# Optimization experiments

Measured on AMD Instinct MI355X. Metric: run time of the kernel, lower is better.

The kernel has to match this reference:

```python
import jax, jax.numpy as jnp
import numpy as np
import math

D_MODEL = 1024
BATCH, SEQ = 8, 2048
EPS_ENT = 1e-10
EPS_LN = 1e-5


def setup_inputs() -> dict:
    key = jax.random.key(0)
    kq, kk, kv, kw = jax.random.split(key, 4)
    query = jax.random.normal(kq, (BATCH, SEQ, D_MODEL), dtype=jnp.float32)
    k_ = jax.random.normal(kk, (BATCH, SEQ, D_MODEL), dtype=jnp.float32)
    v_ = jax.random.normal(kv, (BATCH, SEQ, D_MODEL), dtype=jnp.float32)
    harm_w = jax.random.normal(kw, (D_MODEL, D_MODEL), dtype=jnp.float32) / math.sqrt(D_MODEL)
    harm_b = jnp.zeros((D_MODEL,), dtype=jnp.float32)
    norm_gamma = jnp.ones((D_MODEL,), dtype=jnp.float32)
    norm_beta = jnp.zeros((D_MODEL,), dtype=jnp.float32)
    return {"query": query, "key": k_, "value": v_, "harm_w": harm_w,
            "harm_b": harm_b, "norm_gamma": norm_gamma, "norm_beta": norm_beta}


def reference(query, key, value, harm_w, harm_b, norm_gamma, norm_beta):
    scale = jnp.asarray(math.sqrt(D_MODEL), dtype=query.dtype)
    # scores: [B, Sq, Sk]
    scores = jnp.einsum('bqd,bkd->bqk', query, key) / scale
    attention = jax.nn.softmax(scores, axis=-1)
    # dropout p=0 (eval/deterministic)
    # syntony stat (no-grad in original): normalized mean entropy of attention rows
    entropy = -jnp.sum(attention * jnp.log(attention + EPS_ENT), axis=-1)
    max_entropy = math.log(attention.shape[-1])
    syntony = jnp.clip(1.0 - jnp.mean(entropy) / max_entropy, 0.0, 1.0)
    # output: [B, Sq, D]
    output = jnp.einsum('bqk,bkd->bqd', attention, value)
    # harmonize: linear then syntonic norm (layernorm-style) over feature dim
    h = jnp.einsum('bqd,de->bqe', output, harm_w) + harm_b
    mu = jnp.mean(h, axis=-1, keepdims=True)
    var = jnp.var(h, axis=-1, keepdims=True)
    out = (h - mu) * jax.lax.rsqrt(var + EPS_LN) * norm_gamma + norm_beta
    return out, syntony
```

## Files before the change

kernel.cpp:

```cpp
#include <hip/hip_runtime.h>
#include <math.h>

#define D_MODEL 1024
#define SEQ 2048
#define BATCH 8
#define ROWS (BATCH*SEQ)

typedef __attribute__((ext_vector_type(8))) short bf16x8;
typedef __attribute__((ext_vector_type(4))) float f32x4;

__device__ __forceinline__ unsigned short f2bf(float f) {
  union { float f; unsigned u; } x; x.f = f;
  unsigned r = x.u + 0x7fffu + ((x.u >> 16) & 1u);
  return (unsigned short)(r >> 16);
}

__device__ __forceinline__ void gld16(const unsigned short* g, unsigned short* l) {
  __builtin_amdgcn_global_load_lds(
      (const __attribute__((address_space(1))) unsigned int*)g,
      (__attribute__((address_space(3))) unsigned int*)l, 16, 0, 0);
}

#define BAR() __builtin_amdgcn_s_barrier()
#define LDSOFF(p) ((unsigned)(size_t)(__attribute__((address_space(3))) unsigned short*)(p))

template<int EPI>
__global__ __launch_bounds__(512, 2)
void gemm_b(const unsigned short* __restrict__ A, const unsigned short* __restrict__ B,
            void* __restrict__ Cp, int lda, int ldb, int ldc, int K,
            size_t sA, size_t sB, size_t sC, float scale,
            float* __restrict__ lsum, float* __restrict__ tsum, int lstride,
            const float* __restrict__ bias)
{
  __shared__ __align__(16) unsigned short S[2][2][2][8192];
  const int tid  = threadIdx.x;
  const int lane = tid & 63;
  const int wid  = tid >> 6;
  const int quad = lane >> 4, l16 = lane & 15;
  const int wr = wid >> 2, wc = wid & 3;
  const int m0 = blockIdx.y * 256, n0 = blockIdx.x * 256;
  const int bz = blockIdx.z;

  const int sr = tid >> 2;
  const int u  = ((tid & 3) - (sr >> 1)) & 3;
  const unsigned short* Ag0 = A + (size_t)bz * sA + (size_t)(m0 + sr) * lda + u * 8;
  const unsigned short* Ag1 = Ag0 + (size_t)128 * lda;
  const unsigned short* Bg0 = B + (size_t)bz * sB + (size_t)(n0 + sr) * ldb + u * 8;
  const unsigned short* Bg1 = Bg0 + (size_t)128 * ldb;
  const int ldst = tid * 8;

  f32x4 acc[8][4];
#pragma unroll
  for (int i = 0; i < 8; i++)
#pragma unroll
    for (int j = 0; j < 4; j++) acc[i][j] = (f32x4){0.f, 0.f, 0.f, 0.f};

  const int NT = K >> 6;
  bf16x8 af[4], bfr[4];

#define STG(mat, bufp, ks, koff) do { \
    gld16(((mat) ? Bg0 : Ag0) + (koff), &S[bufp][mat][ks][ldst]); \
    gld16(((mat) ? Bg1 : Ag1) + (koff), &S[bufp][mat][ks][4096 + ldst]); \
  } while (0)

#define LOAD_A(mih, ks, P) do { \
    const int R0 = wr * 128 + (mih) * 64 + l16; \
    const int s = (quad + (R0 >> 1)) & 3; \
    const unsigned offA = LDSOFF(&S[P][0][ks][R0 * 32 + s * 8]); \
    asm volatile("ds_read_b128 %0, %1 offset:0"    : "=v"(af[0]) : "v"(offA)); \
    asm volatile("ds_read_b128 %0, %1 offset:1024" : "=v"(af[1]) : "v"(offA)); \
    asm volatile("ds_read_b128 %0, %1 offset:2048" : "=v"(af[2]) : "v"(offA)); \
    asm volatile("ds_read_b128 %0, %1 offset:3072" : "=v"(af[3]) : "v"(offA)); \
  } while (0)

#define LOAD_B(ks, P) do { \
    const int R0 = wc * 64 + l16; \
    const int s = (quad + (R0 >> 1)) & 3; \
    const unsigned offB = LDSOFF(&S[P][1][ks][R0 * 32 + s * 8]); \
    asm volatile("ds_read_b128 %0, %1 offset:0"    : "=v"(bfr[0]) : "v"(offB)); \
    asm volatile("ds_read_b128 %0, %1 offset:1024" : "=v"(bfr[1]) : "v"(offB)); \
    asm volatile("ds_read_b128 %0, %1 offset:2048" : "=v"(bfr[2]) : "v"(offB)); \
    asm volatile("ds_read_b128 %0, %1 offset:3072" : "=v"(bfr[3]) : "v"(offB)); \
  } while (0)

#define MWAIT() do { \
    asm volatile("s_waitcnt lgkmcnt(0)" ::: "memory"); \
    __builtin_amdgcn_sched_barrier(0); \
  } while (0)

#define MFMA16(mih) do { \
    _Pragma("unroll") \
    for (int i = 0; i < 4; i++) \
    _Pragma("unroll") \
    for (int j = 0; j < 4; j++) \
      acc[(mih) * 4 + i][j] = __builtin_amdgcn_mfma_f32_16x16x32_bf16( \
          af[i], bfr[j], acc[(mih) * 4 + i][j], 0, 0, 0); \
  } while (0)

#define TILE_BODY(P, v) do { \
    const int kHi = ((v) + 1) * 64 + 32; \
    const int kLo = ((v) + 2) * 64; \
     \
    LOAD_A(0, 0, P); LOAD_B(0, P); \
    if ((v) + 1 < NT) STG(0, (P) ^ 1, 1, kHi); \
    BAR(); MWAIT(); \
    __builtin_amdgcn_s_setprio(1); MFMA16(0); __builtin_amdgcn_s_setprio(0); \
    BAR(); \
     \
    LOAD_A(1, 0, P); \
    if ((v) + 1 < NT) STG(1, (P) ^ 1, 1, kHi); \
    BAR(); MWAIT(); \
    __builtin_amdgcn_s_setprio(1); MFMA16(1); __builtin_amdgcn_s_setprio(0); \
    BAR(); \
     \
    LOAD_A(0, 1, P); LOAD_B(1, P); \
    if ((v) + 2 < NT) STG(0, P, 0, kLo); \
    BAR(); MWAIT(); \
    __builtin_amdgcn_s_setprio(1); MFMA16(0); __builtin_amdgcn_s_setprio(0); \
    BAR(); \
     \
    LOAD_A(1, 1, P); \
    if ((v) + 2 < NT) STG(1, P, 0, kLo); \
    BAR(); MWAIT(); \
    __builtin_amdgcn_s_setprio(1); MFMA16(1); __builtin_amdgcn_s_setprio(0); \
     \
    if ((v) + 1 < NT) { \
      if ((v) + 2 < NT) asm volatile("s_waitcnt vmcnt(4)" ::: "memory"); \
      else              asm volatile("s_waitcnt vmcnt(0)" ::: "memory"); \
    } \
    BAR(); \
  } while (0)

  STG(0, 0, 0, 0);  STG(1, 0, 0, 0);
  STG(0, 0, 1, 32); STG(1, 0, 1, 32);
  if (NT > 1) { STG(0, 1, 0, 64); STG(1, 1, 0, 64); }

  if (NT > 1) asm volatile("s_waitcnt vmcnt(4)" ::: "memory");
  else        asm volatile("s_waitcnt vmcnt(0)" ::: "memory");
  BAR();

  for (int v = 0; v < NT; v += 2) {
    TILE_BODY(0, v);
    TILE_BODY(1, v + 1);
  }

#undef TILE_BODY
#undef STG
#undef LOAD_A
#undef LOAD_B
#undef MWAIT
#undef MFMA16

  if constexpr (EPI == 0) {
    unsigned short* C = (unsigned short*)Cp + (size_t)bz * sC;
#pragma unroll
    for (int mi = 0; mi < 8; mi++)
#pragma unroll
      for (int r = 0; r < 4; r++) {
        const int grow = m0 + wr * 128 + mi * 16 + quad * 4 + r;
#pragma unroll
        for (int ni = 0; ni < 4; ni++) {
          const int gcol = n0 + wc * 64 + ni * 16 + l16;
          C[(size_t)grow * ldc + gcol] = f2bf(acc[mi][ni][r]);
        }
      }
  } else if constexpr (EPI == 1) {
    unsigned short* C = (unsigned short*)Cp + (size_t)bz * sC;
#pragma unroll
    for (int mi = 0; mi < 8; mi++)
#pragma unroll
      for (int r = 0; r < 4; r++) {
        const int grow = m0 + wr * 128 + mi * 16 + quad * 4 + r;
        float es = 0.f, ts = 0.f;
#pragma unroll
        for (int ni = 0; ni < 4; ni++) {
          const int gcol = n0 + wc * 64 + ni * 16 + l16;
          float s = acc[mi][ni][r] * scale;
          float e = __expf(s);
          es += e; ts += s * e;
          C[(size_t)grow * ldc + gcol] = f2bf(e);
        }
#pragma unroll
        for (int off = 1; off < 16; off <<= 1) {
          es += __shfl_xor(es, off, 64);
          ts += __shfl_xor(ts, off, 64);
        }
        if (l16 == 0) {
          atomicAdd(&lsum[bz * lstride + grow], es);
          atomicAdd(&tsum[bz * lstride + grow], ts);
        }
      }
  } else {
    float* C = (float*)Cp + (size_t)bz * sC;
#pragma unroll
    for (int mi = 0; mi < 8; mi++)
#pragma unroll
      for (int r = 0; r < 4; r++) {
        const int grow = m0 + wr * 128 + mi * 16 + quad * 4 + r;
        const float linv = 1.0f / lsum[bz * lstride + grow];
#pragma unroll
        for (int ni = 0; ni < 4; ni++) {
          const int gcol = n0 + wc * 64 + ni * 16 + l16;
          C[(size_t)grow * ldc + gcol] = acc[mi][ni][r] * linv + bias[gcol];
        }
      }
  }
}

__global__ __launch_bounds__(256)
void cvt_k(const float* __restrict__ src, unsigned short* __restrict__ dst, int n8)
{
  int stride = gridDim.x * 256;
  for (int i = blockIdx.x * 256 + threadIdx.x; i < n8; i += stride) {
    const float4* s = (const float4*)(src + (size_t)i * 8);
    float4 a = s[0], b = s[1];
    union { unsigned short v[8]; uint4 u; } o;
    o.v[0] = f2bf(a.x); o.v[1] = f2bf(a.y); o.v[2] = f2bf(a.z); o.v[3] = f2bf(a.w);
    o.v[4] = f2bf(b.x); o.v[5] = f2bf(b.y); o.v[6] = f2bf(b.z); o.v[7] = f2bf(b.w);
    *(uint4*)(dst + (size_t)i * 8) = o.u;
  }
}

__global__ __launch_bounds__(256)
void wtr_k(const float* __restrict__ W, unsigned short* __restrict__ WT)
{
  __shared__ float t[32][33];
  int bx = blockIdx.x * 32, by = blockIdx.y * 32;
  int tx = threadIdx.x & 31, ty = threadIdx.x >> 5;
#pragma unroll
  for (int i = 0; i < 32; i += 8)
    t[ty + i][tx] = W[(size_t)(by + ty + i) * D_MODEL + bx + tx];
  __syncthreads();
#pragma unroll
  for (int i = 0; i < 32; i += 8)
    WT[(size_t)(bx + ty + i) * D_MODEL + by + tx] = f2bf(t[tx][ty + i]);
}

__global__ __launch_bounds__(256)
void ln_k(float* __restrict__ out, const float* __restrict__ gamma,
          const float* __restrict__ beta)
{
  const size_t row = blockIdx.x;
  float4* p = (float4*)(out + row * D_MODEL);
  const int tid = threadIdx.x;
  float4 v = p[tid];
  float s  = v.x + v.y + v.z + v.w;
  float sq = v.x * v.x + v.y * v.y + v.z * v.z + v.w * v.w;
#pragma unroll
  for (int off = 1; off < 64; off <<= 1) {
    s  += __shfl_xor(s, off, 64);
    sq += __shfl_xor(sq, off, 64);
  }
  __shared__ float sh[8];
  int wv = tid >> 6, lane = tid & 63;
  if (lane == 0) { sh[wv] = s; sh[4 + wv] = sq; }
  __syncthreads();
  s  = sh[0] + sh[1] + sh[2] + sh[3];
  sq = sh[4] + sh[5] + sh[6] + sh[7];
  float mean = s * (1.f / 1024.f);
  float var  = sq * (1.f / 1024.f) - mean * mean;
  float rstd = rsqrtf(var + 1e-5f);
  float4 g = ((const float4*)gamma)[tid];
  float4 b = ((const float4*)beta)[tid];
  v.x = (v.x - mean) * rstd * g.x + b.x;
  v.y = (v.y - mean) * rstd * g.y + b.y;
  v.z = (v.z - mean) * rstd * g.z + b.z;
  v.w = (v.w - mean) * rstd * g.w + b.w;
  p[tid] = v;
}

__global__ __launch_bounds__(256)
void syn_k(const float* __restrict__ l, const float* __restrict__ t,
           float* __restrict__ out)
{
  float s = 0.f;
  for (int r = threadIdx.x; r < ROWS; r += 256) {
    float lv = l[r];
    s += logf(lv) - t[r] / lv;
  }
#pragma unroll
  for (int off = 1; off < 64; off <<= 1) s += __shfl_xor(s, off, 64);
  __shared__ float sh[4];
  if ((threadIdx.x & 63) == 0) sh[threadIdx.x >> 6] = s;
  __syncthreads();
  if (threadIdx.x == 0) {
    float tot  = sh[0] + sh[1] + sh[2] + sh[3];
    float ment = tot / (float)ROWS;
    float syn  = 1.0f - ment / logf((float)SEQ);
    syn = fminf(fmaxf(syn, 0.f), 1.f);
    out[(size_t)ROWS * D_MODEL] = syn;
  }
}

extern "C" void kernel_launch(void* const* d_in, const int* in_sizes, int n_in,
                              void* d_out, int out_size, void* d_ws, size_t ws_size,
                              hipStream_t stream)
{
  const float* q     = (const float*)d_in[0];
  const float* k     = (const float*)d_in[1];
  const float* v     = (const float*)d_in[2];
  const float* hw    = (const float*)d_in[3];
  const float* hb    = (const float*)d_in[4];
  const float* gamma = (const float*)d_in[5];
  const float* beta  = (const float*)d_in[6];
  float* out = (float*)d_out;

  const size_t MB = 1024ull * 1024ull;
  char* ws = (char*)d_ws;
  unsigned short* P   = (unsigned short*)(ws);
  unsigned short* VWT = (unsigned short*)(ws + 64 * MB);
  float* lsum = (float*)(ws + 96 * MB);
  float* tsum = lsum + ROWS;

  unsigned short* Vb = (unsigned short*)out;
  unsigned short* WT = (unsigned short*)((char*)out + 32 * MB);
  unsigned short* Qb = (unsigned short*)out;
  unsigned short* Kb = (unsigned short*)((char*)out + 32 * MB);

  hipMemsetAsync(lsum, 0, 2 * ROWS * sizeof(float), stream);

  const int n8 = ROWS * D_MODEL / 8;

  cvt_k<<<4096, 256, 0, stream>>>(v, Vb, n8);
  wtr_k<<<dim3(32, 32), 256, 0, stream>>>(hw, WT);
  gemm_b<0><<<dim3(ROWS / 256, D_MODEL / 256, 1), 512, 0, stream>>>(
      WT, Vb, VWT, D_MODEL, D_MODEL, ROWS, D_MODEL,
      0, 0, 0, 1.f, nullptr, nullptr, 0, nullptr);

  cvt_k<<<4096, 256, 0, stream>>>(q, Qb, n8);
  cvt_k<<<4096, 256, 0, stream>>>(k, Kb, n8);
  gemm_b<1><<<dim3(SEQ / 256, SEQ / 256, BATCH), 512, 0, stream>>>(
      Qb, Kb, P, D_MODEL, D_MODEL, SEQ, D_MODEL,
      (size_t)SEQ * D_MODEL, (size_t)SEQ * D_MODEL, (size_t)SEQ * SEQ,
      0.03125f, lsum, tsum, SEQ, nullptr);

  gemm_b<2><<<dim3(D_MODEL / 256, SEQ / 256, BATCH), 512, 0, stream>>>(
      P, VWT, out, SEQ, ROWS, D_MODEL, SEQ,
      (size_t)SEQ * SEQ, (size_t)SEQ, (size_t)SEQ * D_MODEL,
      1.f, lsum, tsum, SEQ, hb);

  ln_k<<<ROWS, 256, 0, stream>>>(out, gamma, beta);
  syn_k<<<1, 256, 0, stream>>>(lsum, tsum, out);
}
```

Measured before the change: 468.3 us.

## Remap workgroups across XCDs and merge GEMM tile phases into two larger steps

Workgroup indices are remapped so consecutive tiles land on the same XCD (round-robin chunking by 8), aiming to improve L2 reuse of shared A/B panels. The tile loop now has two phases per k-tile instead of four. Each phase loads all 8 A fragments and 4 B fragments and issues 32 MFMAs, halving the barrier count. This raises register pressure (8 A fragments held at once) and shifts the global prefetch issue points, which may reduce overlap or risk spills under launch bounds of 512 threads with 2 blocks.

```diff
diff --git a/kernel.cpp b/kernel.cpp
--- a/kernel.cpp
+++ b/kernel.cpp
@@ -38,8 +38,18 @@
   const int wid  = tid >> 6;
   const int quad = lane >> 4, l16 = lane & 15;
   const int wr = wid >> 2, wc = wid & 3;
-  const int m0 = blockIdx.y * 256, n0 = blockIdx.x * 256;
-  const int bz = blockIdx.z;
+
+  int bx = blockIdx.x, by = blockIdx.y, bz = blockIdx.z;
+  {
+    const int nx = gridDim.x, ny = gridDim.y;
+    const int nwg = nx * ny * gridDim.z;
+    const int wg  = bx + nx * (by + ny * bz);
+    const int cpx = nwg >> 3;
+    int idx = (wg & 7) * cpx + (wg >> 3);
+    bx = idx % nx; idx /= nx;
+    by = idx % ny; bz = idx / ny;
+  }
+  const int m0 = by * 256, n0 = bx * 256;
 
   const int sr = tid >> 2;
   const int u  = ((tid & 3) - (sr >> 1)) & 3;
@@ -56,24 +66,28 @@
     for (int j = 0; j < 4; j++) acc[i][j] = (f32x4){0.f, 0.f, 0.f, 0.f};
 
   const int NT = K >> 6;
-  bf16x8 af[4], bfr[4];
+  bf16x8 af[8], bfr[4];
 
 #define STG(mat, bufp, ks, koff) do { \
     gld16(((mat) ? Bg0 : Ag0) + (koff), &S[bufp][mat][ks][ldst]); \
     gld16(((mat) ? Bg1 : Ag1) + (koff), &S[bufp][mat][ks][4096 + ldst]); \
   } while (0)
 
-#define LOAD_A(mih, ks, P) do { \
-    const int R0 = wr * 128 + (mih) * 64 + l16; \
+#define LOAD_A8(ks, P) do { \
+    const int R0 = wr * 128 + l16; \
     const int s = (quad + (R0 >> 1)) & 3; \
     const unsigned offA = LDSOFF(&S[P][0][ks][R0 * 32 + s * 8]); \
     asm volatile("ds_read_b128 %0, %1 offset:0"    : "=v"(af[0]) : "v"(offA)); \
     asm volatile("ds_read_b128 %0, %1 offset:1024" : "=v"(af[1]) : "v"(offA)); \
     asm volatile("ds_read_b128 %0, %1 offset:2048" : "=v"(af[2]) : "v"(offA)); \
     asm volatile("ds_read_b128 %0, %1 offset:3072" : "=v"(af[3]) : "v"(offA)); \
-  } while (0)
-
-#define LOAD_B(ks, P) do { \
+    asm volatile("ds_read_b128 %0, %1 offset:4096" : "=v"(af[4]) : "v"(offA)); \
+    asm volatile("ds_read_b128 %0, %1 offset:5120" : "=v"(af[5]) : "v"(offA)); \
+    asm volatile("ds_read_b128 %0, %1 offset:6144" : "=v"(af[6]) : "v"(offA)); \
+    asm volatile("ds_read_b128 %0, %1 offset:7168" : "=v"(af[7]) : "v"(offA)); \
+  } while (0)
+
+#define LOAD_B4(ks, P) do { \
     const int R0 = wc * 64 + l16; \
     const int s = (quad + (R0 >> 1)) & 3; \
     const unsigned offB = LDSOFF(&S[P][1][ks][R0 * 32 + s * 8]); \
@@ -88,41 +102,29 @@
     __builtin_amdgcn_sched_barrier(0); \
   } while (0)
 
-#define MFMA16(mih) do { \
+#define MFMA32() do { \
     _Pragma("unroll") \
-    for (int i = 0; i < 4; i++) \
+    for (int i = 0; i < 8; i++) \
     _Pragma("unroll") \
     for (int j = 0; j < 4; j++) \
-      acc[(mih) * 4 + i][j] = __builtin_amdgcn_mfma_f32_16x16x32_bf16( \
-          af[i], bfr[j], acc[(mih) * 4 + i][j], 0, 0, 0); \
+      acc[i][j] = __builtin_amdgcn_mfma_f32_16x16x32_bf16( \
+          af[i], bfr[j], acc[i][j], 0, 0, 0); \
   } while (0)
 
 #define TILE_BODY(P, v) do { \
     const int kHi = ((v) + 1) * 64 + 32; \
     const int kLo = ((v) + 2) * 64; \
      \
-    LOAD_A(0, 0, P); LOAD_B(0, P); \
-    if ((v) + 1 < NT) STG(0, (P) ^ 1, 1, kHi); \
+    LOAD_A8(0, P); LOAD_B4(0, P); \
+    if ((v) + 1 < NT) { STG(0, (P) ^ 1, 1, kHi); STG(1, (P) ^ 1, 1, kHi); } \
     BAR(); MWAIT(); \
-    __builtin_amdgcn_s_setprio(1); MFMA16(0); __builtin_amdgcn_s_setprio(0); \
+    __builtin_amdgcn_s_setprio(1); MFMA32(); __builtin_amdgcn_s_setprio(0); \
     BAR(); \
      \
-    LOAD_A(1, 0, P); \
-    if ((v) + 1 < NT) STG(1, (P) ^ 1, 1, kHi); \
+    LOAD_A8(1, P); LOAD_B4(1, P); \
+    if ((v) + 2 < NT) { STG(0, P, 0, kLo); STG(1, P, 0, kLo); } \
     BAR(); MWAIT(); \
-    __builtin_amdgcn_s_setprio(1); MFMA16(1); __builtin_amdgcn_s_setprio(0); \
-    BAR(); \
-     \
-    LOAD_A(0, 1, P); LOAD_B(1, P); \
-    if ((v) + 2 < NT) STG(0, P, 0, kLo); \
-    BAR(); MWAIT(); \
-    __builtin_amdgcn_s_setprio(1); MFMA16(0); __builtin_amdgcn_s_setprio(0); \
-    BAR(); \
-     \
-    LOAD_A(1, 1, P); \
-    if ((v) + 2 < NT) STG(1, P, 0, kLo); \
-    BAR(); MWAIT(); \
-    __builtin_amdgcn_s_setprio(1); MFMA16(1); __builtin_amdgcn_s_setprio(0); \
+    __builtin_amdgcn_s_setprio(1); MFMA32(); __builtin_amdgcn_s_setprio(0); \
      \
     if ((v) + 1 < NT) { \
       if ((v) + 2 < NT) asm volatile("s_waitcnt vmcnt(4)" ::: "memory"); \
@@ -146,10 +148,10 @@
 
 #undef TILE_BODY
 #undef STG
-#undef LOAD_A
-#undef LOAD_B
+#undef LOAD_A8
+#undef LOAD_B4
 #undef MWAIT
-#undef MFMA16
+#undef MFMA32
 
   if constexpr (EPI == 0) {
     unsigned short* C = (unsigned short*)Cp + (size_t)bz * sC;
```

New measurement: 491.9 us. 1.05x slower.
